# Optimization experiments

Hardware: AMD Instinct MI355X
Metric: run time of the kernel (lower is better)

Reference implementation:

```python
import jax, jax.numpy as jnp
import numpy as np

N_W = 96  # n_workers
N_F = 96  # n_firms


def setup_inputs() -> dict:
    key = jax.random.key(0)
    kw, kf, kr = jax.random.split(key, 3)
    # Each worker ranks the n_firms+1 options (firms + unmatch) with a random permutation,
    # encoded as a one-hot (n_firms+1, n_firms+1) matrix: W[i, j, k] = 1 iff firm j is at rank k.
    pw = jax.vmap(lambda k: jax.random.permutation(k, N_F + 1))(jax.random.split(kw, N_W))
    W = jnp.eye(N_F + 1, dtype=jnp.float32)[pw]                  # (N_W, N_F+1, N_F+1)
    pf = jax.vmap(lambda k: jax.random.permutation(k, N_W + 1))(jax.random.split(kf, N_F))
    F = jnp.eye(N_W + 1, dtype=jnp.float32)[pf]                  # (N_F, N_W+1, N_W+1)
    # R: permutation (dictatorship order) matrix over all workers+firms; column r is one-hot
    # on the agent that dictates in round r.
    perm = jax.random.permutation(kr, N_W + N_F)
    R = jnp.eye(N_W + N_F, dtype=jnp.float32)[perm]              # (N_W+N_F, N_W+N_F)
    return {"W": W, "F": F, "R": R}


def _triangle_window(x):
    # TriangleWindowFunction.forward: x on (0,1], 2-x on (1,2], 0 elsewhere (clamped at 0).
    return jnp.clip(jnp.where(x > 1.0, 2.0 - x, jnp.where(x > 0.0, x, 0.0)), 0.0)


def _find_counterpart(P):
    # first available (rank-first) choice indicator, then map rank -> agent via P.
    first_j = _triangle_window(jnp.cumsum(jnp.sum(P, axis=0)))
    return P @ first_j[:, None]                                  # (n+1, 1)


def _forward(W, F, R):
    n_w, n_f = W.shape[0], F.shape[0]
    dt = W.dtype
    gate_w = jnp.concatenate([jnp.ones((n_f, 1), dt), jnp.zeros((1, 1), dt)])  # zero out unmatch row
    gate_f = jnp.concatenate([jnp.ones((n_w, 1), dt), jnp.zeros((1, 1), dt)])
    zero1 = jnp.zeros((1,), dt)

    def step(carry, ds):
        Wc, Fc, M = carry
        d_w, d_f = ds                                            # (n_w,), (n_f,)
        P_w = jnp.einsum('wij,w->ij', Wc, d_w)                   # dictator-worker's ranking
        P_f = jnp.einsum('fij,f->ij', Fc, d_f)
        c_w = _find_counterpart(P_w)                             # (n_f+1, 1)
        c_f = _find_counterpart(P_f)                             # (n_w+1, 1)
        dw1 = jnp.concatenate([d_w, zero1])                      # (n_w+1,)
        df1 = jnp.concatenate([d_f, zero1])                      # (n_f+1,)
        # matching += M_w + M_f.T
        M = M + dw1[:, None] * c_w[:, 0][None, :] + c_f * df1[None, :]
        # ranking_masks_for_workers[r] has row i = -d_f[i] (0 on unmatch row): equals -df1[:,None].
        # matching_mask_for_workers = -(c_w * gate_w) broadcast across columns.
        Wn = jnp.clip(Wc - c_w * gate_w - df1[:, None], 0.0) * (1.0 - c_f)[:n_w, :, None]
        Fn = jnp.clip(Fc - c_f * gate_f - dw1[:, None], 0.0) * (1.0 - c_w)[:n_f, :, None]
        return (Wn, Fn, M), None

    xs = (R[:n_w].T, R[n_w:].T)                                  # per-round dictator indicators
    M0 = jnp.zeros((n_w + 1, n_f + 1), dt)
    (_, _, M), _ = jax.lax.scan(step, (W, F, M0), xs)
    return M


def reference(W, F, R):
    return _forward(W, F, R)
```

## Files before the change

### kernel.cpp

```cpp
#include <hip/hip_runtime.h>
#include <hip/hip_bf16.h>

#define N_W 96
#define N_F 96
#define NP1 97
#define W_ELEMS (N_W * NP1 * NP1)
#define R_ELEMS ((N_W + N_F) * (N_W + N_F))
#define TOTAL_DECODE (2 * W_ELEMS + R_ELEMS)

__global__ __launch_bounds__(256) void decode_kernel(
    const float* __restrict__ W, const float* __restrict__ F,
    const float* __restrict__ R,
    short* __restrict__ pw, short* __restrict__ pf, short* __restrict__ ord) {
    int idx = blockIdx.x * blockDim.x + threadIdx.x;
    if (idx < W_ELEMS) {
        if (W[idx] > 0.5f) {
            int i = idx / (NP1 * NP1);
            int rem = idx - i * NP1 * NP1;
            int j = rem / NP1;
            int k = rem - j * NP1;
            pw[i * NP1 + k] = (short)j;
        }
    } else if (idx < 2 * W_ELEMS) {
        int e = idx - W_ELEMS;
        if (F[e] > 0.5f) {
            int i = e / (NP1 * NP1);
            int rem = e - i * NP1 * NP1;
            int j = rem / NP1;
            int k = rem - j * NP1;
            pf[i * NP1 + k] = (short)j;
        }
    } else if (idx < TOTAL_DECODE) {
        int e = idx - 2 * W_ELEMS;
        if (R[e] > 0.5f) {
            int a = e / (N_W + N_F);
            int r = e - a * (N_W + N_F);
            ord[r] = (short)a;
        }
    }
}

__global__ __launch_bounds__(256) void sd_kernel(
    const short* __restrict__ pw_g, const short* __restrict__ pf_g,
    const short* __restrict__ ord_g, float* __restrict__ out) {
    __shared__ short s_pw[N_W * NP1];
    __shared__ short s_pf[N_F * NP1];
    __shared__ short s_ord[N_W + N_F];
    __shared__ unsigned char s_m[NP1 * NP1];
    __shared__ unsigned char rem_firm[NP1];
    __shared__ unsigned char rem_work[NP1];
    __shared__ unsigned char zero_f[N_F];
    __shared__ unsigned char zero_w[N_W];

    const int t = threadIdx.x;
    for (int i = t; i < N_W * NP1; i += 256) { s_pw[i] = pw_g[i]; s_pf[i] = pf_g[i]; }
    for (int i = t; i < N_W + N_F; i += 256) s_ord[i] = ord_g[i];
    for (int i = t; i < NP1 * NP1; i += 256) s_m[i] = 0;
    if (t < NP1) { rem_firm[t] = 0; rem_work[t] = 0; }
    if (t < N_W) { zero_w[t] = 0; zero_f[t] = 0; }
    __syncthreads();

    if (t < 64) {
        for (int r = 0; r < N_W + N_F; ++r) {
            int a = s_ord[r];
            if (a < N_W) {
                int w = a;
                rem_work[w] = 1;
                if (!zero_w[w]) {
                    const short* pw = &s_pw[w * NP1];
                    int j1 = pw[t];
                    bool a1 = !rem_firm[j1];
                    bool a2 = false;
                    int t2 = t + 64;
                    if (t2 < NP1) { int j2 = pw[t2]; a2 = !rem_firm[j2]; }
                    unsigned long long m1 = __ballot(a1);
                    unsigned long long m2 = __ballot(a2);
                    int k = m1 ? (__ffsll(m1) - 1) : (64 + __ffsll(m2) - 1);
                    int js = pw[k];
                    s_m[w * NP1 + js] = 1;
                    if (js < N_F) { rem_firm[js] = 1; zero_f[js] = 1; }
                }
            } else {
                int f = a - N_W;
                rem_firm[f] = 1;
                if (!zero_f[f]) {
                    const short* pf = &s_pf[f * NP1];
                    int i1 = pf[t];
                    bool a1 = !rem_work[i1];
                    bool a2 = false;
                    int t2 = t + 64;
                    if (t2 < NP1) { int i2 = pf[t2]; a2 = !rem_work[i2]; }
                    unsigned long long m1 = __ballot(a1);
                    unsigned long long m2 = __ballot(a2);
                    int k = m1 ? (__ffsll(m1) - 1) : (64 + __ffsll(m2) - 1);
                    int is = pf[k];
                    s_m[is * NP1 + f] = 1;
                    if (is < N_W) { rem_work[is] = 1; zero_w[is] = 1; }
                }
            }
        }
    }
    __syncthreads();
    for (int i = t; i < NP1 * NP1; i += 256) out[i] = (float)s_m[i];
}

extern "C" void kernel_launch(void* const* d_in, const int* in_sizes, int n_in,
                              void* d_out, int out_size, void* d_ws, size_t ws_size,
                              hipStream_t stream) {
    const float* W = (const float*)d_in[0];
    const float* F = (const float*)d_in[1];
    const float* R = (const float*)d_in[2];
    float* out = (float*)d_out;

    short* pw = (short*)d_ws;
    short* pf = pw + N_W * NP1;
    short* ord = pf + N_F * NP1;

    int blocks = (TOTAL_DECODE + 255) / 256;
    decode_kernel<<<blocks, 256, 0, stream>>>(W, F, R, pw, pf, ord);
    sd_kernel<<<1, 256, 0, stream>>>(pw, pf, ord, out);
}
```

Before: 51.26 us.

## Vectorize decode and keep serial dictatorship state in wave-uniform bitmasks

The decode kernel now reads float4 vectors and writes each agent's preference list into a packed layout of two 16-bit ranks per 32-bit word, with workers and firms in one array. The serial dictatorship loop keeps the removed and zeroed sets as 64-bit register bitmasks instead of shared-memory byte arrays. It prefetches the next eight agents' packed preferences while the current group is processed, and finds the chosen counterpart with readlane. The output is zero-filled with float4 stores and the at most 192 matches are scattered afterwards, which cuts the latency of the single-wave serial chain at the cost of extra branchless select logic per round.

```diff
diff --git a/kernel.cpp b/kernel.cpp
--- a/kernel.cpp
+++ b/kernel.cpp
@@ -1,107 +1,155 @@
 #include <hip/hip_runtime.h>
 #include <hip/hip_bf16.h>
+#include <stdint.h>
 
 #define N_W 96
 #define N_F 96
+#define NAG 192
 #define NP1 97
 #define W_ELEMS (N_W * NP1 * NP1)
-#define R_ELEMS ((N_W + N_F) * (N_W + N_F))
-#define TOTAL_DECODE (2 * W_ELEMS + R_ELEMS)
+#define R_ELEMS (NAG * NAG)
+#define WB ((W_ELEMS / 4 + 255) / 256)
+#define RB ((R_ELEMS / 4 + 255) / 256)
 
 __global__ __launch_bounds__(256) void decode_kernel(
     const float* __restrict__ W, const float* __restrict__ F,
     const float* __restrict__ R,
-    short* __restrict__ pw, short* __restrict__ pf, short* __restrict__ ord) {
-    int idx = blockIdx.x * blockDim.x + threadIdx.x;
-    if (idx < W_ELEMS) {
-        if (W[idx] > 0.5f) {
-            int i = idx / (NP1 * NP1);
-            int rem = idx - i * NP1 * NP1;
-            int j = rem / NP1;
-            int k = rem - j * NP1;
-            pw[i * NP1 + k] = (short)j;
+    short* __restrict__ ps , short* __restrict__ ord) {
+    int b = blockIdx.x;
+    if (b < 2 * WB) {
+        const float* src = (b < WB) ? W : F;
+        int abase = (b < WB) ? 0 : N_W;
+        int i4 = (b - ((b < WB) ? 0 : WB)) * 256 + threadIdx.x;
+        if (i4 < W_ELEMS / 4) {
+            float4 v = ((const float4*)src)[i4];
+            int base = i4 * 4;
+            #pragma unroll
+            for (int u = 0; u < 4; ++u) {
+                float x = (u == 0) ? v.x : (u == 1) ? v.y : (u == 2) ? v.z : v.w;
+                if (x > 0.5f) {
+                    int idx = base + u;
+                    int a = idx / (NP1 * NP1);
+                    int rem = idx - a * (NP1 * NP1);
+                    int j = rem / NP1;
+                    int k = rem - j * NP1;
+                    int slot = (k < 64) ? (2 * k) : (2 * (k - 64) + 1);
+                    ps[(abase + a) * 128 + slot] = (short)j;
+                }
+            }
         }
-    } else if (idx < 2 * W_ELEMS) {
-        int e = idx - W_ELEMS;
-        if (F[e] > 0.5f) {
-            int i = e / (NP1 * NP1);
-            int rem = e - i * NP1 * NP1;
-            int j = rem / NP1;
-            int k = rem - j * NP1;
-            pf[i * NP1 + k] = (short)j;
-        }
-    } else if (idx < TOTAL_DECODE) {
-        int e = idx - 2 * W_ELEMS;
-        if (R[e] > 0.5f) {
-            int a = e / (N_W + N_F);
-            int r = e - a * (N_W + N_F);
-            ord[r] = (short)a;
+    } else {
+        int i4 = (b - 2 * WB) * 256 + threadIdx.x;
+        if (i4 < R_ELEMS / 4) {
+            float4 v = ((const float4*)R)[i4];
+            int base = i4 * 4;
+            #pragma unroll
+            for (int u = 0; u < 4; ++u) {
+                float x = (u == 0) ? v.x : (u == 1) ? v.y : (u == 2) ? v.z : v.w;
+                if (x > 0.5f) {
+                    int idx = base + u;
+                    int a = idx / NAG;
+                    int r = idx - a * NAG;
+                    ord[r] = (short)a;
+                }
+            }
         }
     }
 }
 
 __global__ __launch_bounds__(256) void sd_kernel(
-    const short* __restrict__ pw_g, const short* __restrict__ pf_g,
-    const short* __restrict__ ord_g, float* __restrict__ out) {
-    __shared__ short s_pw[N_W * NP1];
-    __shared__ short s_pf[N_F * NP1];
-    __shared__ short s_ord[N_W + N_F];
-    __shared__ unsigned char s_m[NP1 * NP1];
-    __shared__ unsigned char rem_firm[NP1];
-    __shared__ unsigned char rem_work[NP1];
-    __shared__ unsigned char zero_f[N_F];
-    __shared__ unsigned char zero_w[N_W];
+    const uint32_t* __restrict__ pk_g, const short* __restrict__ ord_g,
+    float* __restrict__ out) {
+    __shared__ __align__(16) uint32_t s_pk[NAG * 64];
+    __shared__ uint4 s_ordq[24];
+    __shared__ uint32_t s_match[NAG];
 
     const int t = threadIdx.x;
-    for (int i = t; i < N_W * NP1; i += 256) { s_pw[i] = pw_g[i]; s_pf[i] = pf_g[i]; }
-    for (int i = t; i < N_W + N_F; i += 256) s_ord[i] = ord_g[i];
-    for (int i = t; i < NP1 * NP1; i += 256) s_m[i] = 0;
-    if (t < NP1) { rem_firm[t] = 0; rem_work[t] = 0; }
-    if (t < N_W) { zero_w[t] = 0; zero_f[t] = 0; }
+    for (int i = t; i < NAG * 64 / 4; i += 256)
+        ((uint4*)s_pk)[i] = ((const uint4*)pk_g)[i];
+    if (t < 24) s_ordq[t] = ((const uint4*)ord_g)[t];
+    if (t < NAG) s_match[t] = 0xFFFFFFFFu;
     __syncthreads();
 
     if (t < 64) {
-        for (int r = 0; r < N_W + N_F; ++r) {
-            int a = s_ord[r];
-            if (a < N_W) {
-                int w = a;
-                rem_work[w] = 1;
-                if (!zero_w[w]) {
-                    const short* pw = &s_pw[w * NP1];
-                    int j1 = pw[t];
-                    bool a1 = !rem_firm[j1];
-                    bool a2 = false;
-                    int t2 = t + 64;
-                    if (t2 < NP1) { int j2 = pw[t2]; a2 = !rem_firm[j2]; }
-                    unsigned long long m1 = __ballot(a1);
-                    unsigned long long m2 = __ballot(a2);
-                    int k = m1 ? (__ffsll(m1) - 1) : (64 + __ffsll(m2) - 1);
-                    int js = pw[k];
-                    s_m[w * NP1 + js] = 1;
-                    if (js < N_F) { rem_firm[js] = 1; zero_f[js] = 1; }
-                }
-            } else {
-                int f = a - N_W;
-                rem_firm[f] = 1;
-                if (!zero_f[f]) {
-                    const short* pf = &s_pf[f * NP1];
-                    int i1 = pf[t];
-                    bool a1 = !rem_work[i1];
-                    bool a2 = false;
-                    int t2 = t + 64;
-                    if (t2 < NP1) { int i2 = pf[t2]; a2 = !rem_work[i2]; }
-                    unsigned long long m1 = __ballot(a1);
-                    unsigned long long m2 = __ballot(a2);
-                    int k = m1 ? (__ffsll(m1) - 1) : (64 + __ffsll(m2) - 1);
-                    int is = pf[k];
-                    s_m[is * NP1 + f] = 1;
-                    if (is < N_W) { rem_work[is] = 1; zero_w[is] = 1; }
-                }
+        unsigned long long remF_lo = 0, remF_hi = 0, remW_lo = 0, remW_hi = 0;
+        unsigned long long zF_lo = 0, zF_hi = 0, zW_lo = 0, zW_hi = 0;
+
+        auto process = [&](int r, int a_in, uint32_t p) {
+            int a = __builtin_amdgcn_readfirstlane(a_in);
+            bool isW = a < N_W;
+            int aa = isW ? a : (a - N_W);
+            bool lo = aa < 64;
+            unsigned long long sbit = 1ull << (aa & 63);
+            unsigned long long s_lo = lo ? sbit : 0ull;
+            unsigned long long s_hi = lo ? 0ull : sbit;
+            unsigned long long zl = isW ? zW_lo : zF_lo;
+            unsigned long long zh = isW ? zW_hi : zF_hi;
+            bool dead = (((lo ? zl : zh) >> (aa & 63)) & 1ull) != 0;
+            remW_lo |= isW ? s_lo : 0ull;  remW_hi |= isW ? s_hi : 0ull;
+            remF_lo |= isW ? 0ull : s_lo;  remF_hi |= isW ? 0ull : s_hi;
+            unsigned long long o_lo = isW ? remF_lo : remW_lo;
+            unsigned long long o_hi = isW ? remF_hi : remW_hi;
+            int j1 = (int)(p & 0xFFFFu);
+            int j2 = (int)(p >> 16);
+            bool av1 = ((((j1 < 64) ? o_lo : o_hi) >> (j1 & 63)) & 1ull) == 0;
+            bool av2 = (t < 33) && (((((j2 < 64) ? o_lo : o_hi) >> (j2 & 63)) & 1ull) == 0);
+            unsigned long long m1 = __ballot(av1);
+            unsigned long long m2 = __ballot(av2);
+            int k = (m1 != 0) ? (__ffsll((unsigned long long)m1) - 1)
+                              : (63 + __ffsll((unsigned long long)m2));
+            uint32_t pc = (uint32_t)__builtin_amdgcn_readlane((int)p, k & 63);
+            int js = (k < 64) ? (int)(pc & 0xFFFFu) : (int)(pc >> 16);
+            int cell = isW ? (aa * NP1 + js) : (js * NP1 + aa);
+            s_match[r] = dead ? 0xFFFFFFFFu : (uint32_t)cell;
+            bool take = (!dead) && (js < 96);
+            unsigned long long cbit = take ? (1ull << (js & 63)) : 0ull;
+            bool clo = js < 64;
+            unsigned long long c_lo = clo ? cbit : 0ull;
+            unsigned long long c_hi = clo ? 0ull : cbit;
+            remF_lo |= isW ? c_lo : 0ull;  remF_hi |= isW ? c_hi : 0ull;
+            zF_lo   |= isW ? c_lo : 0ull;  zF_hi   |= isW ? c_hi : 0ull;
+            remW_lo |= isW ? 0ull : c_lo;  remW_hi |= isW ? 0ull : c_hi;
+            zW_lo   |= isW ? 0ull : c_lo;  zW_hi   |= isW ? 0ull : c_hi;
+        };
+
+        uint4 oq = s_ordq[0];
+        int ag[8];
+        ag[0] = (int)(oq.x & 0xFFFF); ag[1] = (int)(oq.x >> 16);
+        ag[2] = (int)(oq.y & 0xFFFF); ag[3] = (int)(oq.y >> 16);
+        ag[4] = (int)(oq.z & 0xFFFF); ag[5] = (int)(oq.z >> 16);
+        ag[6] = (int)(oq.w & 0xFFFF); ag[7] = (int)(oq.w >> 16);
+        uint32_t pp[8];
+        #pragma unroll
+        for (int i = 0; i < 8; ++i) pp[i] = s_pk[ag[i] * 64 + t];
+
+        for (int g = 0; g < 24; ++g) {
+            int agn[8] = {0, 0, 0, 0, 0, 0, 0, 0};
+            uint32_t ppn[8] = {0, 0, 0, 0, 0, 0, 0, 0};
+            if (g < 23) {
+                uint4 oqn = s_ordq[g + 1];
+                agn[0] = (int)(oqn.x & 0xFFFF); agn[1] = (int)(oqn.x >> 16);
+                agn[2] = (int)(oqn.y & 0xFFFF); agn[3] = (int)(oqn.y >> 16);
+                agn[4] = (int)(oqn.z & 0xFFFF); agn[5] = (int)(oqn.z >> 16);
+                agn[6] = (int)(oqn.w & 0xFFFF); agn[7] = (int)(oqn.w >> 16);
+                #pragma unroll
+                for (int i = 0; i < 8; ++i) ppn[i] = s_pk[agn[i] * 64 + t];
             }
+            #pragma unroll
+            for (int i = 0; i < 8; ++i) process(g * 8 + i, ag[i], pp[i]);
+            #pragma unroll
+            for (int i = 0; i < 8; ++i) { ag[i] = agn[i]; pp[i] = ppn[i]; }
         }
     }
     __syncthreads();
-    for (int i = t; i < NP1 * NP1; i += 256) out[i] = (float)s_m[i];
+
+    for (int i = t; i < 2352; i += 256)
+        ((float4*)out)[i] = make_float4(0.f, 0.f, 0.f, 0.f);
+    if (t == 0) out[9408] = 0.f;
+    __syncthreads();
+    if (t < NAG) {
+        uint32_t c = s_match[t];
+        if (c != 0xFFFFFFFFu) out[c] = 1.0f;
+    }
 }
 
 extern "C" void kernel_launch(void* const* d_in, const int* in_sizes, int n_in,
@@ -112,11 +160,9 @@
     const float* R = (const float*)d_in[2];
     float* out = (float*)d_out;
 
-    short* pw = (short*)d_ws;
-    short* pf = pw + N_W * NP1;
-    short* ord = pf + N_F * NP1;
+    uint32_t* packed = (uint32_t*)d_ws;
+    short* ord = (short*)((char*)d_ws + NAG * 64 * 4);
 
-    int blocks = (TOTAL_DECODE + 255) / 256;
-    decode_kernel<<<blocks, 256, 0, stream>>>(W, F, R, pw, pf, ord);
-    sd_kernel<<<1, 256, 0, stream>>>(pw, pf, ord, out);
+    decode_kernel<<<2 * WB + RB, 256, 0, stream>>>(W, F, R, (short*)packed, ord);
+    sd_kernel<<<1, 256, 0, stream>>>(packed, ord, out);
 }
```

Measured after the change: 68.23 us. 33.1% more time.
